# Kernel optimization log

Hardware: AMD Instinct MI355X
Metric: run time of the kernel (lower is better)

## Reference

```python
import jax, jax.numpy as jnp
import numpy as np


def setup_inputs() -> dict:
    key = jax.random.key(0)
    k1, k2 = jax.random.split(key)
    N, h, w, c = 512, 64, 64, 32
    X = jax.random.normal(k1, (N, h, w, c), dtype=jnp.float32)       # inducing 'images'
    theta = jax.random.normal(k2, (N, 6), dtype=jnp.float32)         # per-point affine params
    return {"X": X, "theta": theta}


def reference(X, theta):
    # X: (N, h, w, c); theta: (N, 6) -> affine A: (N, 2, 3)
    N, h, w, c = X.shape
    A = theta.reshape(N, 2, 3)

    # Homogeneous target grid (3, h*w) in [-1, 1] coords ('xy' meshgrid as in source).
    Xt, Yt = jnp.meshgrid(jnp.linspace(-1.0, 1.0, w), jnp.linspace(-1.0, 1.0, h))
    Gt = jnp.stack([Xt.ravel(), Yt.ravel(), jnp.ones(h * w, dtype=jnp.float32)])  # (3, HW)

    # Source sampling coordinates per inducing point: (N, 2, HW)
    Gs = jnp.einsum('nij,jk->nik', A, Gt)
    gx = w * (Gs[:, 0, :] + 1.0) / 2.0   # (N, HW)
    gy = h * (Gs[:, 1, :] + 1.0) / 2.0

    X0 = jnp.clip(jnp.floor(gx).astype(jnp.int32), 0, w - 1)
    X1 = jnp.clip(jnp.floor(gx).astype(jnp.int32) + 1, 0, w - 1)
    Y0 = jnp.clip(jnp.floor(gy).astype(jnp.int32), 0, h - 1)
    Y1 = jnp.clip(jnp.floor(gy).astype(jnp.int32) + 1, 0, h - 1)

    # Bilinear weights computed from clipped corner indices (matches source).
    wa = (X1 - gx) * (Y1 - gy)
    wb = (X1 - gx) * (gy - Y0)
    wc = (gx - X0) * (Y1 - gy)
    wd = (gx - X0) * (gy - Y0)

    Sf = X.reshape(N, h * w, c)

    def gather(yi, xi):
        idx = yi * w + xi                                   # (N, HW); clipped so 'wrap' is a no-op
        return jnp.take_along_axis(Sf, idx[..., None], axis=1)  # (N, HW, c)

    T = (wa[..., None] * gather(Y0, X0)
         + wb[..., None] * gather(Y1, X0)
         + wc[..., None] * gather(Y0, X1)
         + wd[..., None] * gather(Y1, X1))
    return T.reshape(N, h, w, c)
```

## Files before the change

### kernel.cpp

```cpp
#include <hip/hip_runtime.h>

#define NIMG 512
#define H 64
#define W 64
#define C 32
#define HW (H * W)
#define TPB 512

typedef _Float16 half8 __attribute__((ext_vector_type(8)));
typedef _Float16 half4v __attribute__((ext_vector_type(4)));

__device__ __forceinline__ int iclamp(int v, int lo, int hi) {
    return v < lo ? lo : (v > hi ? hi : v);
}

__device__ __forceinline__ half8 splat8(_Float16 x) {
    half8 v = {x, x, x, x, x, x, x, x};
    return v;
}

__global__ __launch_bounds__(TPB) void stn_bilinear_lds_kernel(
    const float* __restrict__ X,
    const float* __restrict__ theta,
    float* __restrict__ out)
{
    __shared__ _Float16 s[HW * 8];

    const int b   = blockIdx.x;
    const int xcd = b & 7;
    const int sb  = b >> 3;
    const int oct = sb & 3;
    const int n   = xcd + ((sb >> 2) << 3);
    const int tid = threadIdx.x;

    const float* th = theta + n * 6;
    const double a00 = (double)th[0], a01 = (double)th[1], a02 = (double)th[2];
    const double a10 = (double)th[3], a11 = (double)th[4], a12 = (double)th[5];

    const float* img = X + (size_t)n * (HW * C) + oct * 8;

    for (int it = tid; it < HW * 2; it += TPB) {
        const int p  = it >> 1;
        const int hf = it & 1;
        const float4 v = *(const float4*)(img + (size_t)p * C + hf * 4);
        half4v hv = {( _Float16)v.x, (_Float16)v.y, (_Float16)v.z, (_Float16)v.w};
        *(half4v*)&s[p * 8 + hf * 4] = hv;
    }

    __syncthreads();

    const double step = 2.0 / 63.0;

    float* outb = out + (size_t)n * (HW * C) + oct * 8;

    for (int it = tid; it < HW; it += TPB) {
        const int row = it >> 6;
        const int col = it & 63;

        const double xj = (col == W - 1) ? 1.0 : ((double)col * step - 1.0);
        const double yi = (row == H - 1) ? 1.0 : ((double)row * step - 1.0);

        const double gs0 = (a00 * xj + a01 * yi) + a02;
        const double gs1 = (a10 * xj + a11 * yi) + a12;
        const double gx = (double)W * (gs0 + 1.0) * 0.5;
        const double gy = (double)H * (gs1 + 1.0) * 0.5;

        double fx = floor(gx);
        double fy = floor(gy);
        fx = fmin(fmax(fx, -1.0e6), 1.0e6);
        fy = fmin(fmax(fy, -1.0e6), 1.0e6);
        const int x0i = (int)fx;
        const int y0i = (int)fy;

        const int X0 = iclamp(x0i,     0, W - 1);
        const int X1 = iclamp(x0i + 1, 0, W - 1);
        const int Y0 = iclamp(y0i,     0, H - 1);
        const int Y1 = iclamp(y0i + 1, 0, H - 1);

        float wax = (float)((double)X1 - gx);
        float wbx = (float)(gx - (double)X0);
        float way = (float)((double)Y1 - gy);
        float wby = (float)(gy - (double)Y0);

        if (X0 == X1) { wax = 0.0f; wbx = 0.0f; }
        if (Y0 == Y1) { way = 0.0f; wby = 0.0f; }

        const half8 A  = *(const half8*)&s[(Y0 * W + X0) * 8];
        const half8 Bv = *(const half8*)&s[(Y1 * W + X0) * 8];
        const half8 Cv = *(const half8*)&s[(Y0 * W + X1) * 8];
        const half8 Dv = *(const half8*)&s[(Y1 * W + X1) * 8];

        const half8 vway = splat8((_Float16)way);
        const half8 vwby = splat8((_Float16)wby);
        const half8 vwax = splat8((_Float16)wax);
        const half8 vwbx = splat8((_Float16)wbx);

        const half8 left  = A  * vway + Bv * vwby;
        const half8 right = Cv * vway + Dv * vwby;
        const half8 res   = left * vwax + right * vwbx;

        float rf[8];
#pragma unroll
        for (int k = 0; k < 8; ++k) rf[k] = (float)res[k];

        float* po = outb + (size_t)it * C;
        *(float4*)(po)     = make_float4(rf[0], rf[1], rf[2], rf[3]);
        *(float4*)(po + 4) = make_float4(rf[4], rf[5], rf[6], rf[7]);
    }
}

extern "C" void kernel_launch(void* const* d_in, const int* in_sizes, int n_in,
                              void* d_out, int out_size, void* d_ws, size_t ws_size,
                              hipStream_t stream) {
    const float* X     = (const float*)d_in[0];
    const float* theta = (const float*)d_in[1];
    float* out         = (float*)d_out;

    const int blocks = NIMG * 4;
    hipLaunchKernelGGL(stn_bilinear_lds_kernel, dim3(blocks), dim3(TPB), 0, stream,
                       X, theta, out);
}
```

Baseline: 491.8 us.

## Split into fp16 pack pass and global-gather kernel using workspace

```diff
diff --git a/kernel.cpp b/kernel.cpp
--- a/kernel.cpp
+++ b/kernel.cpp
@@ -5,7 +5,6 @@
 #define W 64
 #define C 32
 #define HW (H * W)
-#define TPB 512
 
 typedef _Float16 half8 __attribute__((ext_vector_type(8)));
 typedef _Float16 half4v __attribute__((ext_vector_type(4)));
@@ -19,6 +18,115 @@
     return v;
 }
 
+__global__ __launch_bounds__(256) void stn_pack_kernel(
+    const float* __restrict__ X, _Float16* __restrict__ Xh)
+{
+    const int b     = blockIdx.x;
+    const int xcd   = b & 7;
+    const int sub   = b >> 3;
+    const int n     = xcd * 64 + (sub >> 4);
+    const int chunk = sub & 15;
+    const int p     = chunk * 256 + threadIdx.x;
+
+    const float* src = X + ((size_t)n * HW + p) * C;
+    float v[32];
+#pragma unroll
+    for (int i = 0; i < 8; ++i)
+        *(float4*)&v[i * 4] = ((const float4*)src)[i];
+
+    _Float16* dst = Xh + (size_t)n * (4 * HW * 8) + (size_t)p * 8;
+#pragma unroll
+    for (int o = 0; o < 4; ++o) {
+        half8 hv;
+#pragma unroll
+        for (int k = 0; k < 8; ++k) hv[k] = (_Float16)v[o * 8 + k];
+        *(half8*)(dst + (size_t)o * (HW * 8)) = hv;
+    }
+}
+
+__global__ __launch_bounds__(256) void stn_gather_kernel(
+    const _Float16* __restrict__ Xh,
+    const float* __restrict__ theta,
+    float* __restrict__ out)
+{
+    const int b     = blockIdx.x;
+    const int xcd   = b & 7;
+    const int sub   = b >> 3;
+    const int n     = xcd * 64 + (sub >> 4);
+    const int chunk = sub & 15;
+    const int p     = chunk * 256 + threadIdx.x;
+    const int row   = p >> 6;
+    const int col   = p & 63;
+
+    const float* th = theta + n * 6;
+    const double a00 = (double)th[0], a01 = (double)th[1], a02 = (double)th[2];
+    const double a10 = (double)th[3], a11 = (double)th[4], a12 = (double)th[5];
+
+    const double step = 2.0 / 63.0;
+    const double xj = (col == W - 1) ? 1.0 : ((double)col * step - 1.0);
+    const double yi = (row == H - 1) ? 1.0 : ((double)row * step - 1.0);
+
+    const double gs0 = (a00 * xj + a01 * yi) + a02;
+    const double gs1 = (a10 * xj + a11 * yi) + a12;
+    const double gx = (double)W * (gs0 + 1.0) * 0.5;
+    const double gy = (double)H * (gs1 + 1.0) * 0.5;
+
+    double fx = floor(gx);
+    double fy = floor(gy);
+    fx = fmin(fmax(fx, -1.0e6), 1.0e6);
+    fy = fmin(fmax(fy, -1.0e6), 1.0e6);
+    const int x0i = (int)fx;
+    const int y0i = (int)fy;
+
+    const int X0 = iclamp(x0i,     0, W - 1);
+    const int X1 = iclamp(x0i + 1, 0, W - 1);
+    const int Y0 = iclamp(y0i,     0, H - 1);
+    const int Y1 = iclamp(y0i + 1, 0, H - 1);
+
+    float wax = (float)((double)X1 - gx);
+    float wbx = (float)(gx - (double)X0);
+    float way = (float)((double)Y1 - gy);
+    float wby = (float)(gy - (double)Y0);
+
+    if (X0 == X1) { wax = 0.0f; wbx = 0.0f; }
+    if (Y0 == Y1) { way = 0.0f; wby = 0.0f; }
+
+    const half8 vway = splat8((_Float16)way);
+    const half8 vwby = splat8((_Float16)wby);
+    const half8 vwax = splat8((_Float16)wax);
+    const half8 vwbx = splat8((_Float16)wbx);
+
+    const _Float16* base = Xh + (size_t)n * (4 * HW * 8);
+    const int iA = (Y0 * W + X0) * 8;
+    const int iB = (Y1 * W + X0) * 8;
+    const int iC = (Y0 * W + X1) * 8;
+    const int iD = (Y1 * W + X1) * 8;
+
+    half8 Av[4], Bv[4], Cv[4], Dv[4];
+#pragma unroll
+    for (int o = 0; o < 4; ++o) {
+        const _Float16* bo = base + (size_t)o * (HW * 8);
+        Av[o] = *(const half8*)(bo + iA);
+        Bv[o] = *(const half8*)(bo + iB);
+        Cv[o] = *(const half8*)(bo + iC);
+        Dv[o] = *(const half8*)(bo + iD);
+    }
+
+    float* po = out + ((size_t)n * HW + p) * C;
+#pragma unroll
+    for (int o = 0; o < 4; ++o) {
+        const half8 left  = Av[o] * vway + Bv[o] * vwby;
+        const half8 right = Cv[o] * vway + Dv[o] * vwby;
+        const half8 res   = left * vwax + right * vwbx;
+        float rf[8];
+#pragma unroll
+        for (int k = 0; k < 8; ++k) rf[k] = (float)res[k];
+        ((float4*)po)[o * 2]     = make_float4(rf[0], rf[1], rf[2], rf[3]);
+        ((float4*)po)[o * 2 + 1] = make_float4(rf[4], rf[5], rf[6], rf[7]);
+    }
+}
+
+#define TPB 512
 __global__ __launch_bounds__(TPB) void stn_bilinear_lds_kernel(
     const float* __restrict__ X,
     const float* __restrict__ theta,
@@ -43,14 +151,13 @@
         const int p  = it >> 1;
         const int hf = it & 1;
         const float4 v = *(const float4*)(img + (size_t)p * C + hf * 4);
-        half4v hv = {( _Float16)v.x, (_Float16)v.y, (_Float16)v.z, (_Float16)v.w};
+        half4v hv = {(_Float16)v.x, (_Float16)v.y, (_Float16)v.z, (_Float16)v.w};
         *(half4v*)&s[p * 8 + hf * 4] = hv;
     }
 
     __syncthreads();
 
     const double step = 2.0 / 63.0;
-
     float* outb = out + (size_t)n * (HW * C) + oct * 8;
 
     for (int it = tid; it < HW; it += TPB) {
@@ -116,7 +223,18 @@
     const float* theta = (const float*)d_in[1];
     float* out         = (float*)d_out;
 
-    const int blocks = NIMG * 4;
-    hipLaunchKernelGGL(stn_bilinear_lds_kernel, dim3(blocks), dim3(TPB), 0, stream,
-                       X, theta, out);
-}
+    const size_t need = (size_t)NIMG * 4 * HW * 8 * sizeof(_Float16);
+
+    if (d_ws != nullptr && ws_size >= need) {
+        _Float16* Xh = (_Float16*)d_ws;
+        const int blocks = NIMG * HW / 256;
+        hipLaunchKernelGGL(stn_pack_kernel, dim3(blocks), dim3(256), 0, stream,
+                           X, Xh);
+        hipLaunchKernelGGL(stn_gather_kernel, dim3(blocks), dim3(256), 0, stream,
+                           Xh, theta, out);
+    } else {
+        const int blocks = NIMG * 4;
+        hipLaunchKernelGGL(stn_bilinear_lds_kernel, dim3(blocks), dim3(TPB), 0,
+                           stream, X, theta, out);
+    }
+}
```

New measurement: 547.1 us. 1.11x slower.
